# Kernel optimization log

Hardware: AMD Instinct MI355X
Metric: run time of the kernel (lower is better)

## Reference

```python
import jax, jax.numpy as jnp
import numpy as np

B, S, D = 4, 2048, 1024
H = 16
HD = D // H  # 64


def setup_inputs() -> dict:
    key = jax.random.key(0)
    ks = jax.random.split(key, 5)
    std = 1.0 / np.sqrt(D)
    return {
        "x": jax.random.normal(ks[0], (B, S, D), dtype=jnp.float32),
        "Wq": jax.random.normal(ks[1], (D, D), dtype=jnp.float32) * std,
        "Wk": jax.random.normal(ks[2], (D, D), dtype=jnp.float32) * std,
        "Wv": jax.random.normal(ks[3], (D, D), dtype=jnp.float32) * std,
        "Wo": jax.random.normal(ks[4], (D, D), dtype=jnp.float32) * std,
        "bo": jnp.zeros((D,), dtype=jnp.float32),
    }


def reference(x, Wq, Wk, Wv, Wo, bo):
    b, n, d_in = x.shape
    q = (x @ Wq).reshape(b, n, H, HD).transpose(0, 2, 1, 3)  # [b,h,n,hd]
    k = (x @ Wk).reshape(b, n, H, HD).transpose(0, 2, 1, 3)
    v = (x @ Wv).reshape(b, n, H, HD).transpose(0, 2, 1, 3)
    scores = jnp.einsum("bhqd,bhkd->bhqk", q, k)  # full NxN, as in original
    causal = jnp.tril(jnp.ones((n, n), dtype=bool))  # True = keep
    scores = jnp.where(causal, scores, -jnp.inf)
    attn = jax.nn.softmax(scores / np.sqrt(HD), axis=-1)
    # dropout p=0.0 -> identity
    ctx = jnp.einsum("bhqk,bhkd->bqhd", attn, v).reshape(b, n, H * HD)
    return ctx @ Wo + bo
```

## Files before the change

### kernel.cpp

```cpp
#include <hip/hip_runtime.h>
#include <math.h>

#define BATCH 4
#define SLEN 2048
#define DMODEL 1024
#define NH 16
#define HD 64
#define MROWS (BATCH * SLEN)
#define QK_LD 2048

typedef __attribute__((ext_vector_type(8))) short short8;
typedef __attribute__((ext_vector_type(4))) float floatx4;

#define AS1 __attribute__((address_space(1)))
#define AS3 __attribute__((address_space(3)))

__device__ inline unsigned short f2bf(float f) {
    union { float f; unsigned u; } a; a.f = f;
    unsigned r = a.u + 0x7fff + ((a.u >> 16) & 1);
    return (unsigned short)(r >> 16);
}

__device__ inline unsigned pack_bf(float lo, float hi) {
    union { float f; unsigned u; } a, b; a.f = lo; b.f = hi;
    return __builtin_amdgcn_perm(b.u + 0x8000u, a.u + 0x8000u, 0x07060302u);
}
__device__ inline unsigned pack_tr(float lo, float hi) {
    union { float f; unsigned u; } a, b; a.f = lo; b.f = hi;
    return __builtin_amdgcn_perm(b.u, a.u, 0x07060302u);
}


__global__ __launch_bounds__(256) void cvt_bf16(const float* __restrict__ src,
                                                short* __restrict__ dst) {
    int i = (blockIdx.x * 256 + threadIdx.x) * 4;
    float4 v = *(const float4*)(src + i);
    unsigned short t0 = f2bf(v.x), t1 = f2bf(v.y), t2 = f2bf(v.z), t3 = f2bf(v.w);
    uint2 o;
    o.x = (unsigned)t0 | ((unsigned)t1 << 16);
    o.y = (unsigned)t2 | ((unsigned)t3 << 16);
    *(uint2*)(dst + i) = o;
}

__global__ __launch_bounds__(256) void cvt_wT4(
    const float* __restrict__ Wq, const float* __restrict__ Wk,
    const float* __restrict__ Wv, const float* __restrict__ Wo,
    short* __restrict__ WqkT, short* __restrict__ WvT, short* __restrict__ WoT)
{
    const float* W; short* Wt; float sc = 1.0f;
    int z = blockIdx.z;
    if (z == 0)      { W = Wq; Wt = WqkT; sc = 0.18033688011112042f; }
    else if (z == 1) { W = Wk; Wt = WqkT + (size_t)DMODEL * DMODEL; }
    else if (z == 2) { W = Wv; Wt = WvT; }
    else             { W = Wo; Wt = WoT; }

    __shared__ float t[32][33];
    int bn = blockIdx.x * 32, bk = blockIdx.y * 32;
    int tx = threadIdx.x & 31, r0 = (threadIdx.x >> 5) * 4;
    #pragma unroll
    for (int i = 0; i < 4; i++)
        t[r0 + i][tx] = W[(size_t)(bk + r0 + i) * DMODEL + bn + tx];
    __syncthreads();
    #pragma unroll
    for (int i = 0; i < 4; i++)
        Wt[(size_t)(bn + r0 + i) * DMODEL + bk + tx] = (short)f2bf(t[tx][r0 + i] * sc);
}

#define TM 128
#define TN 128
#define TK 32

template <int OUT_BF16>
__global__ __launch_bounds__(256) void mfma_gemm(
    const short* __restrict__ A,
    const short* __restrict__ Bt,
    const float* __restrict__ bias,
    void* __restrict__ Cout, int M, int N, int K)
{
    __shared__ short As[2][TM * TK];
    __shared__ short Bs[2][TN * TK];
    int tid = threadIdx.x;
    int m0 = blockIdx.y * TM, n0 = blockIdx.x * TN;
    int l = tid & 63, w = tid >> 6;
    int wm = (w >> 1) * 64, wn = (w & 1) * 64;
    int lr = l & 15, lk = (l >> 4) * 8;

    const short* asrc[2];
    const short* bsrc[2];
    #pragma unroll
    for (int r = 0; r < 2; r++) {
        int c = r * 256 + tid;
        int mm = c >> 2, kk = (c & 3) * 8;
        asrc[r] = A  + (size_t)(m0 + mm) * K + kk;
        bsrc[r] = Bt + (size_t)(n0 + mm) * K + kk;
    }

    floatx4 acc[4][4] = {};

    #pragma unroll
    for (int r = 0; r < 2; r++) {
        int c = r * 256 + tid;
        __builtin_amdgcn_global_load_lds((const AS1 void*)asrc[r],
            (AS3 void*)(&As[0][0] + c * 8), 16, 0, 0);
        __builtin_amdgcn_global_load_lds((const AS1 void*)bsrc[r],
            (AS3 void*)(&Bs[0][0] + c * 8), 16, 0, 0);
        asrc[r] += TK; bsrc[r] += TK;
    }

    int nk = K / TK;
    for (int t = 0; t < nk; t++) {
        int cur = t & 1;
        if (t + 1 < nk) {
            #pragma unroll
            for (int r = 0; r < 2; r++) {
                int c = r * 256 + tid;
                __builtin_amdgcn_global_load_lds((const AS1 void*)asrc[r],
                    (AS3 void*)(&As[cur ^ 1][0] + c * 8), 16, 0, 0);
                __builtin_amdgcn_global_load_lds((const AS1 void*)bsrc[r],
                    (AS3 void*)(&Bs[cur ^ 1][0] + c * 8), 16, 0, 0);
                asrc[r] += TK; bsrc[r] += TK;
            }
            asm volatile("s_waitcnt vmcnt(4)" ::: "memory");
        } else {
            asm volatile("s_waitcnt vmcnt(0)" ::: "memory");
        }
        __builtin_amdgcn_s_barrier();
        __builtin_amdgcn_sched_barrier(0);

        short8 af[4], bg[4];
        #pragma unroll
        for (int i = 0; i < 4; i++) {
            af[i] = *(const short8*)(&As[cur][0] + (wm + i * 16 + lr) * TK + lk);
            bg[i] = *(const short8*)(&Bs[cur][0] + (wn + i * 16 + lr) * TK + lk);
        }
        #pragma unroll
        for (int mi = 0; mi < 4; mi++)
            #pragma unroll
            for (int ni = 0; ni < 4; ni++)
                acc[mi][ni] = __builtin_amdgcn_mfma_f32_16x16x32_bf16(
                    af[mi], bg[ni], acc[mi][ni], 0, 0, 0);

        __builtin_amdgcn_sched_barrier(0);
        __builtin_amdgcn_s_barrier();
    }

    int rbase = (l >> 4) * 4, cbase = l & 15;
    if (OUT_BF16) {
        short* C = (short*)Cout;
        #pragma unroll
        for (int mi = 0; mi < 4; mi++)
            #pragma unroll
            for (int r = 0; r < 4; r++) {
                int row = m0 + wm + mi * 16 + rbase + r;
                #pragma unroll
                for (int ni = 0; ni < 4; ni++) {
                    int col = n0 + wn + ni * 16 + cbase;
                    C[(size_t)row * N + col] = (short)f2bf(acc[mi][ni][r]);
                }
            }
    } else {
        float* C = (float*)Cout;
        #pragma unroll
        for (int mi = 0; mi < 4; mi++)
            #pragma unroll
            for (int r = 0; r < 4; r++) {
                int row = m0 + wm + mi * 16 + rbase + r;
                #pragma unroll
                for (int ni = 0; ni < 4; ni++) {
                    int col = n0 + wn + ni * 16 + cbase;
                    C[(size_t)row * N + col] = acc[mi][ni][r] + bias[col];
                }
            }
    }
}

#define PSTR 72

__global__ __launch_bounds__(256, 4) void fa_mfma(
    const short* __restrict__ QK, const short* __restrict__ VtT,
    short* __restrict__ ctx)
{
    __shared__ __align__(16) short Ks[2][2][64][32];
    __shared__ __align__(16) short Vs[2][2][64][32];
    __shared__ __align__(16) short Ps[4][16][PSTR];

    int tid = threadIdx.x;
    int l = tid & 63, w = tid >> 6;
    int lr = l & 15, lg = l >> 4;
    int bh = blockIdx.x;
    int b = bh >> 4, h = bh & 15;
    int qt = 31 - blockIdx.y;
    int q0 = qt * 64;

    const short* Qbase = QK + (size_t)b * SLEN * QK_LD + h * HD;
    const short* Kbase = Qbase + 1024;
    const short* Vbase = VtT + (size_t)h * HD * MROWS + b * SLEN;

    int xoff = (lg ^ ((lr >> 1) & 3)) * 8;

    short8 ones;
    #pragma unroll
    for (int j = 0; j < 8; j++) ones[j] = (short)0x3F80;

    int qrow = q0 + w * 16 + lr;

    short8 qf[2];
    #pragma unroll
    for (int kk = 0; kk < 2; kk++)
        qf[kk] = *(const short8*)(Qbase + (size_t)qrow * QK_LD + kk * 32 + lg * 8);

    const short* ksrc[2];
    const short* vsrc[2];
    #pragma unroll
    for (int r2 = 0; r2 < 2; r2++) {
        int cc = r2 * 256 + tid;
        int kh = cc >> 8, rr = (cc >> 2) & 63;
        int q = (cc & 3) ^ ((rr >> 1) & 3);
        ksrc[r2] = Kbase + (size_t)rr * QK_LD + kh * 32 + q * 8;
        vsrc[r2] = Vbase + (size_t)rr * MROWS + kh * 32 + q * 8;
    }

    floatx4 O[4] = {};
    floatx4 accL = {};

    #pragma unroll
    for (int r2 = 0; r2 < 2; r2++) {
        int cc = r2 * 256 + tid;
        __builtin_amdgcn_global_load_lds((const AS1 void*)ksrc[r2],
            (AS3 void*)(&Ks[0][0][0][0] + cc * 8), 16, 0, 0);
        __builtin_amdgcn_global_load_lds((const AS1 void*)vsrc[r2],
            (AS3 void*)(&Vs[0][0][0][0] + cc * 8), 16, 0, 0);
        ksrc[r2] += (size_t)64 * QK_LD;
        vsrc[r2] += 64;
    }

    for (int kt = 0; kt <= qt; kt++) {
        int cur = kt & 1;
        int k0 = kt * 64;
        if (kt < qt) {
            #pragma unroll
            for (int r2 = 0; r2 < 2; r2++) {
                int cc = r2 * 256 + tid;
                __builtin_amdgcn_global_load_lds((const AS1 void*)ksrc[r2],
                    (AS3 void*)(&Ks[cur ^ 1][0][0][0] + cc * 8), 16, 0, 0);
                __builtin_amdgcn_global_load_lds((const AS1 void*)vsrc[r2],
                    (AS3 void*)(&Vs[cur ^ 1][0][0][0] + cc * 8), 16, 0, 0);
                ksrc[r2] += (size_t)64 * QK_LD;
                vsrc[r2] += 64;
            }
            asm volatile("s_waitcnt vmcnt(4)" ::: "memory");
        } else {
            asm volatile("s_waitcnt vmcnt(0)" ::: "memory");
        }
        __builtin_amdgcn_s_barrier();
        __builtin_amdgcn_sched_barrier(0);

        floatx4 s4[4] = {};
        #pragma unroll
        for (int kk = 0; kk < 2; kk++)
            #pragma unroll
            for (int t = 0; t < 4; t++) {
                short8 kf = *(const short8*)(&Ks[cur][kk][t * 16 + lr][xoff]);
                s4[t] = __builtin_amdgcn_mfma_f32_16x16x32_bf16(kf, qf[kk], s4[t], 0, 0, 0);
            }

        if (kt == qt) {
            #pragma unroll
            for (int t = 0; t < 4; t++)
                #pragma unroll
                for (int r = 0; r < 4; r++)
                    if (k0 + t * 16 + lg * 4 + r > qrow) s4[t][r] = -INFINITY;
        }

        #pragma unroll
        for (int t = 0; t < 4; t++) {
            float p0 = __builtin_amdgcn_exp2f(s4[t][0]);
            float p1 = __builtin_amdgcn_exp2f(s4[t][1]);
            float p2 = __builtin_amdgcn_exp2f(s4[t][2]);
            float p3 = __builtin_amdgcn_exp2f(s4[t][3]);
            uint2 pk;
            pk.x = pack_tr(p0, p1);
            pk.y = pack_tr(p2, p3);
            *(uint2*)(&Ps[w][lr][t * 16 + lg * 4]) = pk;
        }

        #pragma unroll
        for (int kk = 0; kk < 2; kk++) {
            short8 pf = *(const short8*)(&Ps[w][lr][kk * 32 + lg * 8]);
            accL = __builtin_amdgcn_mfma_f32_16x16x32_bf16(ones, pf, accL, 0, 0, 0);
            #pragma unroll
            for (int dt = 0; dt < 4; dt++) {
                short8 vf = *(const short8*)(&Vs[cur][kk][dt * 16 + lr][xoff]);
                O[dt] = __builtin_amdgcn_mfma_f32_16x16x32_bf16(vf, pf, O[dt], 0, 0, 0);
            }
        }

        __builtin_amdgcn_sched_barrier(0);
        __builtin_amdgcn_s_barrier();
    }

    float linv = 1.f / accL[0];
    short* crow = ctx + ((size_t)b * SLEN + qrow) * DMODEL + h * HD;
    #pragma unroll
    for (int dt = 0; dt < 4; dt++) {
        uint2 pk;
        pk.x = pack_bf(O[dt][0] * linv, O[dt][1] * linv);
        pk.y = pack_bf(O[dt][2] * linv, O[dt][3] * linv);
        *(uint2*)(crow + dt * 16 + lg * 4) = pk;
    }
}

extern "C" void kernel_launch(void* const* d_in, const int* in_sizes, int n_in,
                              void* d_out, int out_size, void* d_ws, size_t ws_size,
                              hipStream_t stream) {
    const float* x  = (const float*)d_in[0];
    const float* Wq = (const float*)d_in[1];
    const float* Wk = (const float*)d_in[2];
    const float* Wv = (const float*)d_in[3];
    const float* Wo = (const float*)d_in[4];
    const float* bo = (const float*)d_in[5];
    float* out = (float*)d_out;

    const size_t tsz = (size_t)MROWS * DMODEL;
    const size_t wsz = (size_t)DMODEL * DMODEL;

    short* xb    = (short*)d_ws;
    short* WqkT  = xb + tsz;
    short* WvT   = WqkT + 2 * wsz;
    short* WoT   = WvT + wsz;
    short* QKb   = WoT + wsz;
    short* VtT   = QKb + 2 * tsz;
    short* Cb    = VtT + tsz;

    cvt_bf16<<<(int)(tsz / (256 * 4)), 256, 0, stream>>>(x, xb);
    cvt_wT4<<<dim3(32, 32, 4), 256, 0, stream>>>(Wq, Wk, Wv, Wo, WqkT, WvT, WoT);

    mfma_gemm<1><<<dim3(2048 / TN, MROWS / TM), 256, 0, stream>>>(
        xb, WqkT, nullptr, QKb, MROWS, 2048, DMODEL);
    mfma_gemm<1><<<dim3(MROWS / TN, DMODEL / TM), 256, 0, stream>>>(
        WvT, xb, nullptr, VtT, DMODEL, MROWS, DMODEL);

    fa_mfma<<<dim3(BATCH * NH, 32), 256, 0, stream>>>(QKb, VtT, Cb);

    mfma_gemm<0><<<dim3(DMODEL / TN, MROWS / TM), 256, 0, stream>>>(
        Cb, WoT, bo, out, MROWS, DMODEL, DMODEL);
}
```

Baseline: 266.6 us.

## Merge conversion and QKV GEMM launches; single-buffer attention K/V tiles

Combines the x conversion and weight transpose-conversion kernels into one launch, and merges the QK and V projection GEMMs into one grid that dispatches on block index. This removes launch gaps and tail effects between small kernels. The attention kernel also drops its double-buffered async K/V prefetch in favour of a single buffer loaded between two __syncthreads. That halves K/V LDS use but exposes global-load latency on every key tile, with no overlap with the MFMA work.

```diff
diff --git a/kernel.cpp b/kernel.cpp
--- a/kernel.cpp
+++ b/kernel.cpp
@@ -30,40 +30,45 @@
     return __builtin_amdgcn_perm(b.u, a.u, 0x07060302u);
 }
 
-
-__global__ __launch_bounds__(256) void cvt_bf16(const float* __restrict__ src,
-                                                short* __restrict__ dst) {
-    int i = (blockIdx.x * 256 + threadIdx.x) * 4;
-    float4 v = *(const float4*)(src + i);
-    unsigned short t0 = f2bf(v.x), t1 = f2bf(v.y), t2 = f2bf(v.z), t3 = f2bf(v.w);
-    uint2 o;
-    o.x = (unsigned)t0 | ((unsigned)t1 << 16);
-    o.y = (unsigned)t2 | ((unsigned)t3 << 16);
-    *(uint2*)(dst + i) = o;
-}
-
-__global__ __launch_bounds__(256) void cvt_wT4(
+__global__ __launch_bounds__(256) void cvt_all(
+    const float* __restrict__ x,
     const float* __restrict__ Wq, const float* __restrict__ Wk,
     const float* __restrict__ Wv, const float* __restrict__ Wo,
+    short* __restrict__ xb,
     short* __restrict__ WqkT, short* __restrict__ WvT, short* __restrict__ WoT)
 {
-    const float* W; short* Wt; float sc = 1.0f;
-    int z = blockIdx.z;
-    if (z == 0)      { W = Wq; Wt = WqkT; sc = 0.18033688011112042f; }
-    else if (z == 1) { W = Wk; Wt = WqkT + (size_t)DMODEL * DMODEL; }
-    else if (z == 2) { W = Wv; Wt = WvT; }
-    else             { W = Wo; Wt = WoT; }
-
-    __shared__ float t[32][33];
-    int bn = blockIdx.x * 32, bk = blockIdx.y * 32;
-    int tx = threadIdx.x & 31, r0 = (threadIdx.x >> 5) * 4;
-    #pragma unroll
-    for (int i = 0; i < 4; i++)
-        t[r0 + i][tx] = W[(size_t)(bk + r0 + i) * DMODEL + bn + tx];
-    __syncthreads();
-    #pragma unroll
-    for (int i = 0; i < 4; i++)
-        Wt[(size_t)(bn + r0 + i) * DMODEL + bk + tx] = (short)f2bf(t[tx][r0 + i] * sc);
+    int bid = blockIdx.x;
+    if (bid < 8192) {
+        int i = (bid * 256 + threadIdx.x) * 4;
+        float4 v = *(const float4*)(x + i);
+        unsigned short t0 = f2bf(v.x), t1 = f2bf(v.y), t2 = f2bf(v.z), t3 = f2bf(v.w);
+        uint2 o;
+        o.x = (unsigned)t0 | ((unsigned)t1 << 16);
+        o.y = (unsigned)t2 | ((unsigned)t3 << 16);
+        *(uint2*)(xb + i) = o;
+    } else {
+        bid -= 8192;
+        int z = bid >> 10;
+        int inner = bid & 1023;
+        int bxi = inner & 31, byi = inner >> 5;
+
+        const float* W; short* Wt; float sc = 1.0f;
+        if (z == 0)      { W = Wq; Wt = WqkT; sc = 0.18033688011112042f; }
+        else if (z == 1) { W = Wk; Wt = WqkT + (size_t)DMODEL * DMODEL; }
+        else if (z == 2) { W = Wv; Wt = WvT; }
+        else             { W = Wo; Wt = WoT; }
+
+        __shared__ float t[32][33];
+        int bn = bxi * 32, bk = byi * 32;
+        int tx = threadIdx.x & 31, r0 = (threadIdx.x >> 5) * 4;
+        #pragma unroll
+        for (int i = 0; i < 4; i++)
+            t[r0 + i][tx] = W[(size_t)(bk + r0 + i) * DMODEL + bn + tx];
+        __syncthreads();
+        #pragma unroll
+        for (int i = 0; i < 4; i++)
+            Wt[(size_t)(bn + r0 + i) * DMODEL + bk + tx] = (short)f2bf(t[tx][r0 + i] * sc);
+    }
 }
 
 #define TM 128
@@ -71,16 +76,15 @@
 #define TK 32
 
 template <int OUT_BF16>
-__global__ __launch_bounds__(256) void mfma_gemm(
+__device__ __forceinline__ void gemm_body(
     const short* __restrict__ A,
     const short* __restrict__ Bt,
     const float* __restrict__ bias,
-    void* __restrict__ Cout, int M, int N, int K)
+    void* __restrict__ Cout, int N, int K, int m0, int n0)
 {
     __shared__ short As[2][TM * TK];
     __shared__ short Bs[2][TN * TK];
     int tid = threadIdx.x;
-    int m0 = blockIdx.y * TM, n0 = blockIdx.x * TN;
     int l = tid & 63, w = tid >> 6;
     int wm = (w >> 1) * 64, wn = (w & 1) * 64;
     int lr = l & 15, lk = (l >> 4) * 8;
@@ -174,14 +178,42 @@
     }
 }
 
+template <int OUT_BF16>
+__global__ __launch_bounds__(256) void mfma_gemm(
+    const short* __restrict__ A, const short* __restrict__ Bt,
+    const float* __restrict__ bias, void* __restrict__ Cout,
+    int M, int N, int K)
+{
+    int m0 = blockIdx.y * TM, n0 = blockIdx.x * TN;
+    gemm_body<OUT_BF16>(A, Bt, bias, Cout, N, K, m0, n0);
+}
+
+__global__ __launch_bounds__(256) void qkv_gemm(
+    const short* __restrict__ xb, const short* __restrict__ WqkT,
+    const short* __restrict__ WvT, short* __restrict__ QKb,
+    short* __restrict__ VtT)
+{
+    const short* A; const short* Bt; short* C; int N, m0, n0;
+    int bid = blockIdx.x;
+    if (bid < 1024) {
+        A = xb; Bt = WqkT; C = QKb; N = 2048;
+        m0 = (bid >> 4) * TM; n0 = (bid & 15) * TN;
+    } else {
+        int r = bid - 1024;
+        A = WvT; Bt = xb; C = VtT; N = MROWS;
+        m0 = (r >> 6) * TM; n0 = (r & 63) * TN;
+    }
+    gemm_body<1>(A, Bt, nullptr, C, N, DMODEL, m0, n0);
+}
+
 #define PSTR 72
 
 __global__ __launch_bounds__(256, 4) void fa_mfma(
     const short* __restrict__ QK, const short* __restrict__ VtT,
     short* __restrict__ ctx)
 {
-    __shared__ __align__(16) short Ks[2][2][64][32];
-    __shared__ __align__(16) short Vs[2][2][64][32];
+    __shared__ __align__(16) short Ks[2][64][32];
+    __shared__ __align__(16) short Vs[2][64][32];
     __shared__ __align__(16) short Ps[4][16][PSTR];
 
     int tid = threadIdx.x;
@@ -223,44 +255,29 @@
     floatx4 O[4] = {};
     floatx4 accL = {};
 
-    #pragma unroll
-    for (int r2 = 0; r2 < 2; r2++) {
-        int cc = r2 * 256 + tid;
-        __builtin_amdgcn_global_load_lds((const AS1 void*)ksrc[r2],
-            (AS3 void*)(&Ks[0][0][0][0] + cc * 8), 16, 0, 0);
-        __builtin_amdgcn_global_load_lds((const AS1 void*)vsrc[r2],
-            (AS3 void*)(&Vs[0][0][0][0] + cc * 8), 16, 0, 0);
-        ksrc[r2] += (size_t)64 * QK_LD;
-        vsrc[r2] += 64;
-    }
-
     for (int kt = 0; kt <= qt; kt++) {
-        int cur = kt & 1;
         int k0 = kt * 64;
-        if (kt < qt) {
-            #pragma unroll
-            for (int r2 = 0; r2 < 2; r2++) {
-                int cc = r2 * 256 + tid;
-                __builtin_amdgcn_global_load_lds((const AS1 void*)ksrc[r2],
-                    (AS3 void*)(&Ks[cur ^ 1][0][0][0] + cc * 8), 16, 0, 0);
-                __builtin_amdgcn_global_load_lds((const AS1 void*)vsrc[r2],
-                    (AS3 void*)(&Vs[cur ^ 1][0][0][0] + cc * 8), 16, 0, 0);
-                ksrc[r2] += (size_t)64 * QK_LD;
-                vsrc[r2] += 64;
-            }
-            asm volatile("s_waitcnt vmcnt(4)" ::: "memory");
-        } else {
-            asm volatile("s_waitcnt vmcnt(0)" ::: "memory");
-        }
-        __builtin_amdgcn_s_barrier();
-        __builtin_amdgcn_sched_barrier(0);
+        __syncthreads();
+        #pragma unroll
+        for (int r2 = 0; r2 < 2; r2++) {
+            int cc = r2 * 256 + tid;
+            __builtin_amdgcn_global_load_lds(
+                (const AS1 void*)ksrc[r2],
+                (AS3 void*)(&Ks[0][0][0] + cc * 8), 16, 0, 0);
+            __builtin_amdgcn_global_load_lds(
+                (const AS1 void*)vsrc[r2],
+                (AS3 void*)(&Vs[0][0][0] + cc * 8), 16, 0, 0);
+            ksrc[r2] += (size_t)64 * QK_LD;
+            vsrc[r2] += 64;
+        }
+        __syncthreads();
 
         floatx4 s4[4] = {};
         #pragma unroll
         for (int kk = 0; kk < 2; kk++)
             #pragma unroll
             for (int t = 0; t < 4; t++) {
-                short8 kf = *(const short8*)(&Ks[cur][kk][t * 16 + lr][xoff]);
+                short8 kf = *(const short8*)(&Ks[kk][t * 16 + lr][xoff]);
                 s4[t] = __builtin_amdgcn_mfma_f32_16x16x32_bf16(kf, qf[kk], s4[t], 0, 0, 0);
             }
 
@@ -290,13 +307,10 @@
             accL = __builtin_amdgcn_mfma_f32_16x16x32_bf16(ones, pf, accL, 0, 0, 0);
             #pragma unroll
             for (int dt = 0; dt < 4; dt++) {
-                short8 vf = *(const short8*)(&Vs[cur][kk][dt * 16 + lr][xoff]);
+                short8 vf = *(const short8*)(&Vs[kk][dt * 16 + lr][xoff]);
                 O[dt] = __builtin_amdgcn_mfma_f32_16x16x32_bf16(vf, pf, O[dt], 0, 0, 0);
             }
         }
-
-        __builtin_amdgcn_sched_barrier(0);
-        __builtin_amdgcn_s_barrier();
     }
 
     float linv = 1.f / accL[0];
@@ -332,13 +346,9 @@
     short* VtT   = QKb + 2 * tsz;
     short* Cb    = VtT + tsz;
 
-    cvt_bf16<<<(int)(tsz / (256 * 4)), 256, 0, stream>>>(x, xb);
-    cvt_wT4<<<dim3(32, 32, 4), 256, 0, stream>>>(Wq, Wk, Wv, Wo, WqkT, WvT, WoT);
-
-    mfma_gemm<1><<<dim3(2048 / TN, MROWS / TM), 256, 0, stream>>>(
-        xb, WqkT, nullptr, QKb, MROWS, 2048, DMODEL);
-    mfma_gemm<1><<<dim3(MROWS / TN, DMODEL / TM), 256, 0, stream>>>(
-        WvT, xb, nullptr, VtT, DMODEL, MROWS, DMODEL);
+    cvt_all<<<12288, 256, 0, stream>>>(x, Wq, Wk, Wv, Wo, xb, WqkT, WvT, WoT);
+
+    qkv_gemm<<<1536, 256, 0, stream>>>(xb, WqkT, WvT, QKb, VtT);
 
     fa_mfma<<<dim3(BATCH * NH, 32), 256, 0, stream>>>(QKb, VtT, Cb);
 
```

Result: faster. 240.4 us (-9.8%).
